# Optimization experiments

Measured on AMD Instinct MI355X. Metric: run time of the kernel, lower is better.

Reference implementation:

```python
import jax, jax.numpy as jnp
import numpy as np

B, Q, K = 4, 128, 1024
DQ, DK, DV, H = 512, 512, 512, 256
NEG_INF = -1e6


def setup_inputs() -> dict:
    key = jax.random.key(0)
    ks = jax.random.split(key, 6)
    queries = jax.random.normal(ks[0], (B, Q, DQ), dtype=jnp.float32)
    keys = jax.random.normal(ks[1], (B, K, DK), dtype=jnp.float32)
    values = jax.random.normal(ks[2], (B, K, DV), dtype=jnp.float32)
    valid_lens = jax.random.randint(ks[3], (B,), 1, K + 1, dtype=jnp.int32)
    # Learned params (Dense use_bias=False): W_q [DQ,H], W_k [DK,H], w_v [H] (Dense(1) squeezed)
    Wq = jax.random.normal(ks[4], (DQ, H), dtype=jnp.float32) / np.sqrt(DQ)
    Wk = jax.random.normal(ks[5], (DK, H), dtype=jnp.float32) / np.sqrt(DK)
    wv = jax.random.normal(jax.random.fold_in(key, 7), (H,), dtype=jnp.float32) / np.sqrt(H)
    return {"queries": queries, "keys": keys, "values": values,
            "valid_lens": valid_lens, "Wq": Wq, "Wk": Wk, "wv": wv}


def reference(queries, keys, values, valid_lens, Wq, Wk, wv):
    q = queries @ Wq                       # [B,Q,H]
    k = keys @ Wk                          # [B,K,H]
    feats = jnp.tanh(q[:, :, None, :] + k[:, None, :, :])   # [B,Q,K,H]
    scores = jnp.einsum('bqkh,h->bqk', feats, wv)            # [B,Q,K]
    mask = jnp.arange(scores.shape[-1]) < valid_lens[:, None, None]  # [B,1,K]
    scores = jnp.where(mask, scores, NEG_INF)
    attn = jax.nn.softmax(scores, axis=-1)                   # [B,Q,K]
    # dropout is identity at inference
    return attn @ values                                     # [B,Q,DV]
```

## Files before the change

kernel.cpp:

```cpp
#include <hip/hip_runtime.h>

#define Bn 4
#define Qn 128
#define Kn 1024
#define Dn 512
#define Hn 256

__device__ __forceinline__ float fast_tanh(float x) {
    float e = __expf(2.0f * x);
    return 1.0f - 2.0f * __builtin_amdgcn_rcpf(1.0f + e);
}

#define PBK 64

__global__ __launch_bounds__(512, 4) void proj_kernel(
    const float* __restrict__ queries, const float* __restrict__ keys,
    const float* __restrict__ Wq, const float* __restrict__ Wk,
    const int* __restrict__ valid_lens,
    float* __restrict__ proj0, float* __restrict__ proj1)
{
    const int blk = blockIdx.x;
    const int kc = blk & 1;
    const int nt = (blk >> 1) & 3;
    const int mt = blk >> 3;
    const int t = threadIdx.x;
    const float* Asrc; const float* W;
    int m0, drow;
    if (mt < 8) {
        m0 = mt * 64;
        drow = m0;
        Asrc = queries; W = Wq;
    } else {
        int r0 = (mt - 8) * 64;
        int b = r0 >> 10;
        if ((r0 & 1023) >= valid_lens[b]) return;
        m0 = r0;
        drow = 512 + r0;
        Asrc = keys; W = Wk;
    }
    const int n0 = nt * 64;
    const int k0 = kc * 256;
    float* Dst = (kc ? proj1 : proj0) + (size_t)drow * Hn;

    __shared__ float s_a[PBK][68];
    __shared__ float s_b[PBK][64];

    const int tt   = t & 255;
    const int kh   = t >> 8;
    const int trow = tt >> 4;
    const int tcol = tt & 15;
    const int kklo = kh << 5;

    const int lrow = t >> 4;
    const int lc4  = t & 15;

    float acc[4][4] = {{0.f}};
    float4 ra[2], rb[2];

    #pragma unroll
    for (int i = 0; i < 2; ++i) {
        ra[i] = *(const float4*)(Asrc + (size_t)(m0 + lrow + i * 32) * Dn + k0 + lc4 * 4);
        rb[i] = *(const float4*)(W + (size_t)(k0 + lrow + i * 32) * Hn + n0 + lc4 * 4);
    }

    for (int kt = 0; kt < 4; ++kt) {
        __syncthreads();
        #pragma unroll
        for (int i = 0; i < 2; ++i) {
            int row = lrow + i * 32;
            s_a[lc4 * 4 + 0][row] = ra[i].x;
            s_a[lc4 * 4 + 1][row] = ra[i].y;
            s_a[lc4 * 4 + 2][row] = ra[i].z;
            s_a[lc4 * 4 + 3][row] = ra[i].w;
            *(float4*)&s_b[row][lc4 * 4] = rb[i];
        }
        __syncthreads();
        if (kt < 3) {
            const int d0n = k0 + (kt + 1) * PBK;
            #pragma unroll
            for (int i = 0; i < 2; ++i) {
                ra[i] = *(const float4*)(Asrc + (size_t)(m0 + lrow + i * 32) * Dn + d0n + lc4 * 4);
                rb[i] = *(const float4*)(W + (size_t)(d0n + lrow + i * 32) * Hn + n0 + lc4 * 4);
            }
        }
        #pragma unroll
        for (int kk = 0; kk < 32; ++kk) {
            float4 a4 = *(const float4*)&s_a[kklo + kk][trow * 4];
            float4 b4 = *(const float4*)&s_b[kklo + kk][tcol * 4];
            float a[4] = {a4.x, a4.y, a4.z, a4.w};
            float b[4] = {b4.x, b4.y, b4.z, b4.w};
            #pragma unroll
            for (int i = 0; i < 4; ++i)
                #pragma unroll
                for (int j = 0; j < 4; ++j)
                    acc[i][j] += a[i] * b[j];
        }
    }

    __syncthreads();
    float* red = &s_a[0][0];
    if (kh) {
        #pragma unroll
        for (int i = 0; i < 4; ++i)
            #pragma unroll
            for (int j = 0; j < 4; ++j)
                red[tt * 17 + i * 4 + j] = acc[i][j];
    }
    __syncthreads();
    if (!kh) {
        #pragma unroll
        for (int i = 0; i < 4; ++i) {
            float4 o;
            o.x = acc[i][0] + red[tt * 17 + i * 4 + 0];
            o.y = acc[i][1] + red[tt * 17 + i * 4 + 1];
            o.z = acc[i][2] + red[tt * 17 + i * 4 + 2];
            o.w = acc[i][3] + red[tt * 17 + i * 4 + 3];
            *(float4*)(Dst + (size_t)(trow * 4 + i) * Hn + n0 + tcol * 4) = o;
        }
    }
}

#define SK_KT 16
#define SK_PAD 260

__global__ __launch_bounds__(256) void score_kernel(
    const float* __restrict__ proj0, const float* __restrict__ proj1,
    const float* __restrict__ wv, const int* __restrict__ valid_lens,
    float* __restrict__ escores, float* __restrict__ rowsum)
{
    const int blk = blockIdx.x;
    const int kt = blk & 63;
    const int qt = (blk >> 6) & 31;
    const int b  = blk >> 11;
    const int vlen = valid_lens[b];
    const int k0 = kt * SK_KT;
    if (k0 >= vlen) return;
    const int q0 = qt * 4;
    const int t = threadIdx.x;

    __shared__ float s_k[SK_KT * SK_PAD];
    __shared__ float s_q[4 * Hn];
    __shared__ float s_wv[Hn];

    {
        const float4* k0p = reinterpret_cast<const float4*>(
            proj0 + ((size_t)512 + (size_t)b * Kn + k0) * Hn);
        const float4* k1p = reinterpret_cast<const float4*>(
            proj1 + ((size_t)512 + (size_t)b * Kn + k0) * Hn);
        #pragma unroll
        for (int i = 0; i < 4; ++i) {
            int idx = t + i * 256;
            int row = idx >> 6, c4 = idx & 63;
            float4 a = k0p[idx];
            float4 c = k1p[idx];
            a.x += c.x; a.y += c.y; a.z += c.z; a.w += c.w;
            *reinterpret_cast<float4*>(&s_k[row * SK_PAD + c4 * 4]) = a;
        }
        float4 qa = reinterpret_cast<const float4*>(
            proj0 + ((size_t)b * Qn + q0) * Hn)[t];
        float4 qb = reinterpret_cast<const float4*>(
            proj1 + ((size_t)b * Qn + q0) * Hn)[t];
        qa.x += qb.x; qa.y += qb.y; qa.z += qb.z; qa.w += qb.w;
        reinterpret_cast<float4*>(s_q)[t] = qa;
        if (t < 64)
            reinterpret_cast<float4*>(s_wv)[t] =
                reinterpret_cast<const float4*>(wv)[t];
    }
    __syncthreads();

    const int wave = t >> 6;
    const int lane = t & 63;
    const int kloc = lane & 15;
    const int hq   = lane >> 4;

    const float4* kr = reinterpret_cast<const float4*>(&s_k[kloc * SK_PAD + hq * 64]);
    const float4* qr = reinterpret_cast<const float4*>(&s_q[wave * Hn + hq * 64]);
    const float4* wr = reinterpret_cast<const float4*>(&s_wv[hq * 64]);

    float s = 0.0f;
    #pragma unroll
    for (int i = 0; i < 16; ++i) {
        float4 kv = kr[i];
        float4 qv = qr[i];
        float4 wq = wr[i];
        s += wq.x * fast_tanh(qv.x + kv.x);
        s += wq.y * fast_tanh(qv.y + kv.y);
        s += wq.z * fast_tanh(qv.z + kv.z);
        s += wq.w * fast_tanh(qv.w + kv.w);
    }
    s += __shfl_xor(s, 16, 64);
    s += __shfl_xor(s, 32, 64);

    const int k = k0 + kloc;
    float e = 0.0f;
    if (lane < 16 && k < vlen) {
        e = __expf(s);
        escores[((size_t)b * Qn + q0 + wave) * Kn + k] = e;
    }
    #pragma unroll
    for (int off = 32; off; off >>= 1)
        e += __shfl_xor(e, off, 64);
    if (lane == 0)
        atomicAdd(&rowsum[b * Qn + q0 + wave], e);
}

__global__ __launch_bounds__(256) void av_kernel(
    const float* __restrict__ escores, const float* __restrict__ values,
    const float* __restrict__ rowsum, float* __restrict__ out)
{
    const int blk = blockIdx.x;
    const int kc = blk & 3;
    const int dh = (blk >> 2) & 1;
    const int qt = (blk >> 3) & 15;
    const int b  = blk >> 7;
    const int t = threadIdx.x;
    const int q0 = qt * 8;
    const int kb = kc * 256;
    const int d  = dh * 256 + t;

    __shared__ float s_e[8][256];
    #pragma unroll
    for (int i = 0; i < 2; ++i) {
        int idx = t + i * 256;
        int row = idx >> 6, c4 = idx & 63;
        *(float4*)&s_e[row][c4 * 4] = *(const float4*)(
            escores + ((size_t)(b * Qn + q0 + row)) * Kn + kb + c4 * 4);
    }
    __syncthreads();

    const float* vb = values + ((size_t)b * Kn + kb) * Dn + d;
    float acc[8] = {0.f};
    #pragma unroll 2
    for (int k = 0; k < 256; k += 4) {
        float v0 = vb[(size_t)(k + 0) * Dn];
        float v1 = vb[(size_t)(k + 1) * Dn];
        float v2 = vb[(size_t)(k + 2) * Dn];
        float v3 = vb[(size_t)(k + 3) * Dn];
        #pragma unroll
        for (int j = 0; j < 8; ++j) {
            float4 e4 = *(const float4*)&s_e[j][k];
            acc[j] += e4.x * v0 + e4.y * v1 + e4.z * v2 + e4.w * v3;
        }
    }
    float* op = out + ((size_t)(b * Qn + q0)) * Dn + d;
    #pragma unroll
    for (int j = 0; j < 8; ++j) {
        float inv = __builtin_amdgcn_rcpf(rowsum[b * Qn + q0 + j]);
        atomicAdd(op + (size_t)j * Dn, acc[j] * inv);
    }
}

extern "C" void kernel_launch(void* const* d_in, const int* in_sizes, int n_in,
                              void* d_out, int out_size, void* d_ws, size_t ws_size,
                              hipStream_t stream) {
    const float* queries    = (const float*)d_in[0];
    const float* keys       = (const float*)d_in[1];
    const float* values     = (const float*)d_in[2];
    const int*   valid_lens = (const int*)  d_in[3];
    const float* Wq         = (const float*)d_in[4];
    const float* Wk         = (const float*)d_in[5];
    const float* wv         = (const float*)d_in[6];
    float* out = (float*)d_out;

    const size_t PROJ_F = (size_t)4608 * Hn;
    float* proj0   = (float*)d_ws;
    float* proj1   = proj0 + PROJ_F;
    float* escores = proj1 + PROJ_F;
    float* rowsum  = escores + (size_t)Bn * Qn * Kn;

    hipMemsetAsync(escores, 0, (size_t)(Bn * Qn * Kn + Bn * Qn) * sizeof(float),
                   stream);
    hipMemsetAsync(out, 0, (size_t)Bn * Qn * Dn * sizeof(float), stream);
    proj_kernel<<<576, 512, 0, stream>>>(queries, keys, Wq, Wk, valid_lens,
                                         proj0, proj1);
    score_kernel<<<Bn * 32 * 64, 256, 0, stream>>>(proj0, proj1, wv,
                                                   valid_lens, escores, rowsum);
    av_kernel<<<512, 256, 0, stream>>>(escores, values, rowsum, out);
}
```

Measured before the change: 153.4 us.

## Fold memsets into projection kernel and retile score and AV kernels

The two memsets are removed: the projection kernel now zeroes the output and rowsum, and the AV kernel masks score reads past valid_len instead of relying on a zeroed escores buffer. The score kernel gives each block 32 queries instead of 4, so each wave reuses one key tile across 8 query rows, cutting grid size and redundant key loads. The AV kernel handles 16 queries by 128 keys with float2 value loads and skips key chunks beyond valid_len. The risks are higher register pressure from the larger accumulators and reliance on the zeroing in the first kernel completing before the atomic adds in later kernels, which holds because all launches share one stream.

```diff
diff --git a/kernel.cpp b/kernel.cpp
--- a/kernel.cpp
+++ b/kernel.cpp
@@ -13,17 +13,25 @@
 
 #define PBK 64
 
-__global__ __launch_bounds__(512, 4) void proj_kernel(
+__global__ __launch_bounds__(512) void proj_kernel(
     const float* __restrict__ queries, const float* __restrict__ keys,
     const float* __restrict__ Wq, const float* __restrict__ Wk,
     const int* __restrict__ valid_lens,
-    float* __restrict__ proj0, float* __restrict__ proj1)
+    float* __restrict__ proj0, float* __restrict__ proj1,
+    float* __restrict__ rowsum, float* __restrict__ out)
 {
     const int blk = blockIdx.x;
+    const int t = threadIdx.x;
+
+    if (blk < 128) {
+        float4 z = {0.f, 0.f, 0.f, 0.f};
+        ((float4*)out)[blk * 512 + t] = z;
+        if (blk == 0) rowsum[t] = 0.f;
+    }
+
     const int kc = blk & 1;
     const int nt = (blk >> 1) & 3;
     const int mt = blk >> 3;
-    const int t = threadIdx.x;
     const float* Asrc; const float* W;
     int m0, drow;
     if (mt < 8) {
@@ -120,9 +128,6 @@
     }
 }
 
-#define SK_KT 16
-#define SK_PAD 260
-
 __global__ __launch_bounds__(256) void score_kernel(
     const float* __restrict__ proj0, const float* __restrict__ proj1,
     const float* __restrict__ wv, const int* __restrict__ valid_lens,
@@ -130,123 +135,138 @@
 {
     const int blk = blockIdx.x;
     const int kt = blk & 63;
-    const int qt = (blk >> 6) & 31;
-    const int b  = blk >> 11;
+    const int qp = (blk >> 6) & 3;
+    const int b  = blk >> 8;
     const int vlen = valid_lens[b];
-    const int k0 = kt * SK_KT;
+    const int k0 = kt * 16;
     if (k0 >= vlen) return;
-    const int q0 = qt * 4;
+    const int q0 = qp * 32;
     const int t = threadIdx.x;
 
-    __shared__ float s_k[SK_KT * SK_PAD];
-    __shared__ float s_q[4 * Hn];
+    __shared__ float s_k[16 * 260];
+    __shared__ float s_q[32 * 256];
     __shared__ float s_wv[Hn];
 
     {
-        const float4* k0p = reinterpret_cast<const float4*>(
-            proj0 + ((size_t)512 + (size_t)b * Kn + k0) * Hn);
-        const float4* k1p = reinterpret_cast<const float4*>(
-            proj1 + ((size_t)512 + (size_t)b * Kn + k0) * Hn);
+        const float4* k0p = (const float4*)(proj0 + ((size_t)(512 + b * Kn + k0)) * Hn);
+        const float4* k1p = (const float4*)(proj1 + ((size_t)(512 + b * Kn + k0)) * Hn);
         #pragma unroll
         for (int i = 0; i < 4; ++i) {
             int idx = t + i * 256;
             int row = idx >> 6, c4 = idx & 63;
-            float4 a = k0p[idx];
-            float4 c = k1p[idx];
+            float4 a = k0p[idx], c = k1p[idx];
             a.x += c.x; a.y += c.y; a.z += c.z; a.w += c.w;
-            *reinterpret_cast<float4*>(&s_k[row * SK_PAD + c4 * 4]) = a;
-        }
-        float4 qa = reinterpret_cast<const float4*>(
-            proj0 + ((size_t)b * Qn + q0) * Hn)[t];
-        float4 qb = reinterpret_cast<const float4*>(
-            proj1 + ((size_t)b * Qn + q0) * Hn)[t];
-        qa.x += qb.x; qa.y += qb.y; qa.z += qb.z; qa.w += qb.w;
-        reinterpret_cast<float4*>(s_q)[t] = qa;
-        if (t < 64)
-            reinterpret_cast<float4*>(s_wv)[t] =
-                reinterpret_cast<const float4*>(wv)[t];
-    }
-    __syncthreads();
-
-    const int wave = t >> 6;
-    const int lane = t & 63;
-    const int kloc = lane & 15;
-    const int hq   = lane >> 4;
-
-    const float4* kr = reinterpret_cast<const float4*>(&s_k[kloc * SK_PAD + hq * 64]);
-    const float4* qr = reinterpret_cast<const float4*>(&s_q[wave * Hn + hq * 64]);
-    const float4* wr = reinterpret_cast<const float4*>(&s_wv[hq * 64]);
-
-    float s = 0.0f;
-    #pragma unroll
+            *(float4*)&s_k[row * 260 + c4 * 4] = a;
+        }
+        const float4* q0p = (const float4*)(proj0 + ((size_t)(b * Qn + q0)) * Hn);
+        const float4* q1p = (const float4*)(proj1 + ((size_t)(b * Qn + q0)) * Hn);
+        #pragma unroll
+        for (int i = 0; i < 8; ++i) {
+            int idx = t + i * 256;
+            float4 a = q0p[idx], c = q1p[idx];
+            a.x += c.x; a.y += c.y; a.z += c.z; a.w += c.w;
+            ((float4*)s_q)[idx] = a;
+        }
+        if (t < 64) ((float4*)s_wv)[t] = ((const float4*)wv)[t];
+    }
+    __syncthreads();
+
+    const int w = t >> 6, lane = t & 63;
+    const int kloc = lane & 15, hq = lane >> 4;
+    const float4* kr = (const float4*)&s_k[kloc * 260 + hq * 64];
+    const float4* wr = (const float4*)&s_wv[hq * 64];
+    const float*  qb = &s_q[(size_t)(w * 8) * 256 + hq * 64];
+
+    float acc[8] = {0.f, 0.f, 0.f, 0.f, 0.f, 0.f, 0.f, 0.f};
+    #pragma unroll 4
     for (int i = 0; i < 16; ++i) {
         float4 kv = kr[i];
-        float4 qv = qr[i];
         float4 wq = wr[i];
-        s += wq.x * fast_tanh(qv.x + kv.x);
-        s += wq.y * fast_tanh(qv.y + kv.y);
-        s += wq.z * fast_tanh(qv.z + kv.z);
-        s += wq.w * fast_tanh(qv.w + kv.w);
-    }
-    s += __shfl_xor(s, 16, 64);
-    s += __shfl_xor(s, 32, 64);
-
+        #pragma unroll
+        for (int qr = 0; qr < 8; ++qr) {
+            float4 qv = *(const float4*)&qb[qr * 256 + i * 4];
+            acc[qr] += wq.x * fast_tanh(qv.x + kv.x)
+                     + wq.y * fast_tanh(qv.y + kv.y)
+                     + wq.z * fast_tanh(qv.z + kv.z)
+                     + wq.w * fast_tanh(qv.w + kv.w);
+        }
+    }
     const int k = k0 + kloc;
-    float e = 0.0f;
-    if (lane < 16 && k < vlen) {
-        e = __expf(s);
-        escores[((size_t)b * Qn + q0 + wave) * Kn + k] = e;
-    }
-    #pragma unroll
-    for (int off = 32; off; off >>= 1)
-        e += __shfl_xor(e, off, 64);
-    if (lane == 0)
-        atomicAdd(&rowsum[b * Qn + q0 + wave], e);
+    #pragma unroll
+    for (int qr = 0; qr < 8; ++qr) {
+        float s = acc[qr];
+        s += __shfl_xor(s, 16, 64);
+        s += __shfl_xor(s, 32, 64);
+        float e = 0.f;
+        if (lane < 16 && k < vlen) {
+            e = __expf(s);
+            escores[((size_t)(b * Qn + q0 + w * 8 + qr)) * Kn + k] = e;
+        }
+        e += __shfl_xor(e, 8, 64);
+        e += __shfl_xor(e, 4, 64);
+        e += __shfl_xor(e, 2, 64);
+        e += __shfl_xor(e, 1, 64);
+        if (lane == 0)
+            atomicAdd(&rowsum[b * Qn + q0 + w * 8 + qr], e);
+    }
 }
 
 __global__ __launch_bounds__(256) void av_kernel(
     const float* __restrict__ escores, const float* __restrict__ values,
-    const float* __restrict__ rowsum, float* __restrict__ out)
+    const float* __restrict__ rowsum, const int* __restrict__ valid_lens,
+    float* __restrict__ out)
 {
     const int blk = blockIdx.x;
-    const int kc = blk & 3;
-    const int dh = (blk >> 2) & 1;
-    const int qt = (blk >> 3) & 15;
-    const int b  = blk >> 7;
+    const int kc = blk & 7;
+    const int qt = (blk >> 3) & 7;
+    const int b  = blk >> 6;
+    const int vlen = valid_lens[b];
+    const int kb = kc * 128;
+    if (kb >= vlen) return;
+    const int q0 = qt * 16;
     const int t = threadIdx.x;
-    const int q0 = qt * 8;
-    const int kb = kc * 256;
-    const int d  = dh * 256 + t;
-
-    __shared__ float s_e[8][256];
+
+    __shared__ float s_e[16 * 128];
     #pragma unroll
     for (int i = 0; i < 2; ++i) {
         int idx = t + i * 256;
-        int row = idx >> 6, c4 = idx & 63;
-        *(float4*)&s_e[row][c4 * 4] = *(const float4*)(
-            escores + ((size_t)(b * Qn + q0 + row)) * Kn + kb + c4 * 4);
-    }
-    __syncthreads();
-
-    const float* vb = values + ((size_t)b * Kn + kb) * Dn + d;
-    float acc[8] = {0.f};
+        int row = idx >> 5, c4 = idx & 31;
+        const float* esrc = escores + ((size_t)(b * Qn + q0 + row)) * Kn + kb + c4 * 4;
+        int kbase = kb + c4 * 4;
+        float4 ev;
+        ev.x = (kbase + 0 < vlen) ? esrc[0] : 0.f;
+        ev.y = (kbase + 1 < vlen) ? esrc[1] : 0.f;
+        ev.z = (kbase + 2 < vlen) ? esrc[2] : 0.f;
+        ev.w = (kbase + 3 < vlen) ? esrc[3] : 0.f;
+        *(float4*)&s_e[row * 128 + c4 * 4] = ev;
+    }
+    __syncthreads();
+
+    const int d0 = t * 2;
+    const float* vb = values + ((size_t)(b * Kn + kb)) * Dn + d0;
+    float accx[16], accy[16];
+    #pragma unroll
+    for (int j = 0; j < 16; ++j) { accx[j] = 0.f; accy[j] = 0.f; }
+
     #pragma unroll 2
-    for (int k = 0; k < 256; k += 4) {
-        float v0 = vb[(size_t)(k + 0) * Dn];
-        float v1 = vb[(size_t)(k + 1) * Dn];
-        float v2 = vb[(size_t)(k + 2) * Dn];
-        float v3 = vb[(size_t)(k + 3) * Dn];
-        #pragma unroll
-        for (int j = 0; j < 8; ++j) {
-            float4 e4 = *(const float4*)&s_e[j][k];
-            acc[j] += e4.x * v0 + e4.y * v1 + e4.z * v2 + e4.w * v3;
-        }
-    }
-    float* op = out + ((size_t)(b * Qn + q0)) * Dn + d;
-    #pragma unroll
-    for (int j = 0; j < 8; ++j) {
+    for (int k = 0; k < 128; k += 4) {
+        float2 v0 = *(const float2*)&vb[(size_t)(k + 0) * Dn];
+        float2 v1 = *(const float2*)&vb[(size_t)(k + 1) * Dn];
+        float2 v2 = *(const float2*)&vb[(size_t)(k + 2) * Dn];
+        float2 v3 = *(const float2*)&vb[(size_t)(k + 3) * Dn];
+        #pragma unroll
+        for (int j = 0; j < 16; ++j) {
+            float4 e4 = *(const float4*)&s_e[j * 128 + k];
+            accx[j] += e4.x * v0.x + e4.y * v1.x + e4.z * v2.x + e4.w * v3.x;
+            accy[j] += e4.x * v0.y + e4.y * v1.y + e4.z * v2.y + e4.w * v3.y;
+        }
+    }
+    float* op = out + ((size_t)(b * Qn + q0)) * Dn + d0;
+    #pragma unroll
+    for (int j = 0; j < 16; ++j) {
         float inv = __builtin_amdgcn_rcpf(rowsum[b * Qn + q0 + j]);
-        atomicAdd(op + (size_t)j * Dn, acc[j] * inv);
+        atomicAdd(op + (size_t)j * Dn + 0, accx[j] * inv);
+        atomicAdd(op + (size_t)j * Dn + 1, accy[j] * inv);
     }
 }
 
@@ -268,12 +288,10 @@
     float* escores = proj1 + PROJ_F;
     float* rowsum  = escores + (size_t)Bn * Qn * Kn;
 
-    hipMemsetAsync(escores, 0, (size_t)(Bn * Qn * Kn + Bn * Qn) * sizeof(float),
-                   stream);
-    hipMemsetAsync(out, 0, (size_t)Bn * Qn * Dn * sizeof(float), stream);
     proj_kernel<<<576, 512, 0, stream>>>(queries, keys, Wq, Wk, valid_lens,
-                                         proj0, proj1);
-    score_kernel<<<Bn * 32 * 64, 256, 0, stream>>>(proj0, proj1, wv,
-                                                   valid_lens, escores, rowsum);
-    av_kernel<<<512, 256, 0, stream>>>(escores, values, rowsum, out);
-}
+                                         proj0, proj1, rowsum, out);
+    score_kernel<<<1024, 256, 0, stream>>>(proj0, proj1, wv, valid_lens,
+                                           escores, rowsum);
+    av_kernel<<<256, 256, 0, stream>>>(escores, values, rowsum, valid_lens,
+                                       out);
+}
```

Result: slower. 168.2 us (+9.7%).
